# Kernel optimization log

Hardware: AMD Instinct MI355X
Metric: run time of the kernel (lower is better)

The kernel has to match this reference:

```python
import jax, jax.numpy as jnp
import numpy as np

WIDTH = 96
MODES = 42
LAYERS = 4
GROUPS = 6  # max(1, min(8, 96 // 16))
EPS = 1e-5
RESIDUAL_SCALE = 0.5


def _coord_grid(B, H, W, dtype):
    y = jnp.linspace(-1.0, 1.0, H, dtype=dtype)
    x = jnp.linspace(-1.0, 1.0, W, dtype=dtype)
    yy, xx = jnp.meshgrid(y, x, indexing='ij')
    grid = jnp.stack([xx, yy], axis=0)  # (2,H,W)
    return jnp.broadcast_to(grid[None], (B, 2, H, W))


def _spectral_conv(x, w):
    # x: (B,C,H,W) real; w: (Ci,Co,M,M,2) real
    B, C, H, W = x.shape
    xf = jnp.fft.rfft2(x)  # (B,C,H,W//2+1) complex
    Hm = min(MODES, H)
    Wm = min(MODES, W // 2 + 1)
    wc = (w[..., 0] + 1j * w[..., 1])[:, :, :Hm, :Wm]
    of = jnp.einsum('bihw,iohw->bohw', xf[:, :, :Hm, :Wm], wc)
    out_ft = jnp.zeros((B, w.shape[1], H, W // 2 + 1), dtype=of.dtype)
    out_ft = out_ft.at[:, :, :Hm, :Wm].set(of)
    return jnp.fft.irfft2(out_ft, s=(H, W))


def _conv1x1(x, w, b):
    # w: (Cout, Cin), b: (Cout,)
    return jnp.einsum('bihw,oi->bohw', x, w) + b[None, :, None, None]


def _depthwise3x3(x, w, b):
    # w: (C,1,3,3)
    y = jax.lax.conv_general_dilated(
        x, w, window_strides=(1, 1), padding=((1, 1), (1, 1)),
        dimension_numbers=('NCHW', 'OIHW', 'NCHW'),
        feature_group_count=x.shape[1])
    return y + b[None, :, None, None]


def _group_norm(x, g, b):
    B, C, H, W = x.shape
    xg = x.reshape(B, GROUPS, C // GROUPS, H, W)
    mean = jnp.mean(xg, axis=(2, 3, 4), keepdims=True)
    var = jnp.var(xg, axis=(2, 3, 4), keepdims=True)
    xn = ((xg - mean) * jax.lax.rsqrt(var + EPS)).reshape(B, C, H, W)
    return xn * g[None, :, None, None] + b[None, :, None, None]


def setup_inputs() -> dict:
    key = jax.random.key(0)
    ks = jax.random.split(key, 16)
    B, H, W = 8, 256, 256
    in_ch = 3 + 1 + 2
    scale = 1.0 / (WIDTH * WIDTH)
    inp = {
        'upsampled': jax.random.uniform(ks[0], (B, 3, H, W), dtype=jnp.float32),
        'noise': 0.1 * jax.random.normal(ks[1], (B, 1, H, W), dtype=jnp.float32),
        'in_proj_w': jax.random.normal(ks[2], (WIDTH, in_ch), dtype=jnp.float32) * (1.0 / np.sqrt(in_ch)),
        'in_proj_b': jnp.zeros((WIDTH,), dtype=jnp.float32),
        'spec_w': scale * jax.random.normal(ks[3], (WIDTH, WIDTH, MODES, MODES, 2), dtype=jnp.float32),
        'dense_w': jax.random.normal(ks[4], (LAYERS, WIDTH, WIDTH), dtype=jnp.float32) * (1.0 / np.sqrt(WIDTH)),
        'dense_b': jnp.zeros((LAYERS, WIDTH), dtype=jnp.float32),
        'local_w': jax.random.normal(ks[5], (LAYERS, WIDTH, 1, 3, 3), dtype=jnp.float32) * (1.0 / 3.0),
        'local_b': jnp.zeros((LAYERS, WIDTH), dtype=jnp.float32),
        'norm_g': jnp.ones((LAYERS, WIDTH), dtype=jnp.float32),
        'norm_b': jnp.zeros((LAYERS, WIDTH), dtype=jnp.float32),
        'out_proj_w': jax.random.normal(ks[6], (3, WIDTH), dtype=jnp.float32) * (1.0 / np.sqrt(WIDTH)),
        'out_proj_b': jnp.zeros((3,), dtype=jnp.float32),
    }
    return inp


def reference(upsampled, noise, in_proj_w, in_proj_b, spec_w, dense_w, dense_b,
              local_w, local_b, norm_g, norm_b, out_proj_w, out_proj_b):
    B, _, H, W = upsampled.shape
    grid = _coord_grid(B, H, W, upsampled.dtype)
    x = jnp.concatenate([upsampled, noise, grid], axis=1)
    x = jax.nn.gelu(_conv1x1(x, in_proj_w, in_proj_b), approximate=False)
    for l in range(LAYERS):
        delta = (_spectral_conv(x, spec_w)
                 + _conv1x1(x, dense_w[l], dense_b[l])
                 + _depthwise3x3(x, local_w[l], local_b[l]))
        x = x + RESIDUAL_SCALE * delta
        x = _group_norm(x, norm_g[l], norm_b[l])
        x = jax.nn.gelu(x, approximate=False)
    residual = _conv1x1(x, out_proj_w, out_proj_b)
    return jnp.clip(upsampled + residual, 0.0, 1.0)
```

## Files before the change

kernel.cpp:

```cpp
#include <hip/hip_runtime.h>
#include <math.h>

#define NHW 65536
#define PADM 1792
#define PI2 6.283185307179586f

__device__ __forceinline__ float gelu_f(float v) {
    return 0.5f * v * (1.0f + erff(v * 0.7071067811865476f));
}

__global__ void k_tables(float* __restrict__ D1, float* __restrict__ T1c, float* __restrict__ T1s,
                         float* __restrict__ T2c, float* __restrict__ T2s) {
    int idx = blockIdx.x * 256 + threadIdx.x;
    if (idx < 256 * 48) {
        int n = idx / 48, k = idx % 48;
        float ang = PI2 * (float)((n * k) & 255) / 256.0f;
        float s, c;
        sincosf(ang, &s, &c);
        D1[n * 96 + 2 * k] = c;
        D1[n * 96 + 2 * k + 1] = -s;
        T1c[n * 48 + k] = c;
        T1s[n * 48 + k] = s;
    }
    if (idx < 42 * 256) {
        int k = idx / 256, n = idx % 256;
        float ang = PI2 * (float)((n * k) & 255) / 256.0f;
        float s, c;
        sincosf(ang, &s, &c);
        T2c[idx] = c;
        T2s[idx] = s;
    }
}

__global__ void k_nrm_init(float2* __restrict__ nrm, int n) {
    int i = blockIdx.x * 256 + threadIdx.x;
    if (i < n) nrm[i] = make_float2(1.0f, 0.0f);
}

__global__ void __launch_bounds__(256) k_in(const float* __restrict__ up, const float* __restrict__ noise,
                                            const float* __restrict__ w, const float* __restrict__ bias,
                                            float* __restrict__ A, int b0) {
    __shared__ float ws_[96 * 6];
    __shared__ float bs_[96];
    int t = threadIdx.x;
    for (int i = t; i < 96 * 6; i += 256) ws_[i] = w[i];
    if (t < 96) bs_[t] = bias[t];
    __syncthreads();
    int br = blockIdx.x >> 8, h = blockIdx.x & 255;
    int b = b0 + br;
    float v0 = up[((size_t)(b * 3 + 0) * 256 + h) * 256 + t];
    float v1 = up[((size_t)(b * 3 + 1) * 256 + h) * 256 + t];
    float v2 = up[((size_t)(b * 3 + 2) * 256 + h) * 256 + t];
    float v3 = noise[((size_t)b * 256 + h) * 256 + t];
    float v4 = -1.0f + 2.0f * (float)t / 255.0f;
    float v5 = -1.0f + 2.0f * (float)h / 255.0f;
    size_t base = (size_t)br * 96 * NHW + (size_t)h * 256 + t;
    for (int o = 0; o < 96; o++) {
        const float* wo = ws_ + o * 6;
        float acc = bs_[o];
        acc = fmaf(v0, wo[0], acc); acc = fmaf(v1, wo[1], acc); acc = fmaf(v2, wo[2], acc);
        acc = fmaf(v3, wo[3], acc); acc = fmaf(v4, wo[4], acc); acc = fmaf(v5, wo[5], acc);
        A[base + (size_t)o * NHW] = acc;
    }
}

__global__ void __launch_bounds__(256) k_s1(const float* __restrict__ A, const float2* __restrict__ nrm,
                                            const float* __restrict__ D1, float* __restrict__ rz) {
    __shared__ float Xl[32][132];
    __shared__ float Dl[32][100];
    int t = threadIdx.x;
    int row0 = blockIdx.x * 128;
    int bc = blockIdx.x >> 1;
    float2 nv = nrm[bc];
    int tn = t % 16, tm = t / 16;
    int r0 = tn * 8, c0 = tm * 6;
    float acc[8][6] = {};
    for (int kc = 0; kc < 256; kc += 32) {
        __syncthreads();
#pragma unroll
        for (int it = 0; it < 4; it++) {
            int slot = t + 256 * it;
            int r = slot >> 3, j4 = (slot & 7) * 4;
            float4 g = *(const float4*)&A[(size_t)(row0 + r) * 256 + kc + j4];
            Xl[j4 + 0][r] = gelu_f(fmaf(g.x, nv.x, nv.y));
            Xl[j4 + 1][r] = gelu_f(fmaf(g.y, nv.x, nv.y));
            Xl[j4 + 2][r] = gelu_f(fmaf(g.z, nv.x, nv.y));
            Xl[j4 + 3][r] = gelu_f(fmaf(g.w, nv.x, nv.y));
        }
#pragma unroll
        for (int it = 0; it < 3; it++) {
            int slot = t + 256 * it;
            int rr = slot / 24, c4 = (slot % 24) * 4;
            *(float4*)&Dl[rr][c4] = *(const float4*)&D1[(size_t)(kc + rr) * 96 + c4];
        }
        __syncthreads();
        for (int k = 0; k < 32; k++) {
            float a[8], d[6];
#pragma unroll
            for (int i = 0; i < 8; i++) a[i] = Xl[k][r0 + i];
#pragma unroll
            for (int j = 0; j < 6; j++) d[j] = Dl[k][c0 + j];
#pragma unroll
            for (int i = 0; i < 8; i++)
#pragma unroll
                for (int j = 0; j < 6; j++) acc[i][j] = fmaf(a[i], d[j], acc[i][j]);
        }
    }
#pragma unroll
    for (int i = 0; i < 8; i++) {
        size_t row = row0 + r0 + i;
#pragma unroll
        for (int j = 0; j < 6; j++) {
            int col = c0 + j;
            if (col < 84) rz[row * 84 + col] = acc[i][j];
        }
    }
}

__global__ void __launch_bounds__(256) k_s2(const float* __restrict__ r1, const float* __restrict__ T1c,
                                            const float* __restrict__ T1s, float* __restrict__ xf) {
    int bc = blockIdx.x;
    int t = threadIdx.x;
    __shared__ float rl[32][88];
    __shared__ float tcl[32][48], tsl[32][48];
    int tkh = t / 11, tkw = t % 11;
    bool act = (t < 231);
    int kh0 = tkh * 2, kw0 = tkw * 4;
    float accr[2][4] = {}, acci[2][4] = {};
    const float* rp = r1 + (size_t)bc * 256 * 84;
    for (int hc = 0; hc < 256; hc += 32) {
        __syncthreads();
        for (int f = t; f < 32 * 88; f += 256) {
            int hl = f / 88, m = f % 88;
            rl[hl][m] = (m < 84) ? rp[(size_t)(hc + hl) * 84 + m] : 0.f;
        }
        for (int f = t; f < 32 * 48; f += 256) {
            int hl = f / 48, k = f % 48;
            tcl[hl][k] = T1c[(hc + hl) * 48 + k];
            tsl[hl][k] = T1s[(hc + hl) * 48 + k];
        }
        __syncthreads();
        if (act) {
            for (int hl = 0; hl < 32; hl++) {
                float c0 = tcl[hl][kh0], s0 = tsl[hl][kh0];
                float c1 = tcl[hl][kh0 + 1], s1v = tsl[hl][kh0 + 1];
#pragma unroll
                for (int j = 0; j < 4; j++) {
                    float arr = rl[hl][(kw0 + j) * 2], aii = rl[hl][(kw0 + j) * 2 + 1];
                    accr[0][j] = fmaf(arr, c0, fmaf(aii, s0, accr[0][j]));
                    acci[0][j] = fmaf(aii, c0, fmaf(-arr, s0, acci[0][j]));
                    accr[1][j] = fmaf(arr, c1, fmaf(aii, s1v, accr[1][j]));
                    acci[1][j] = fmaf(aii, c1, fmaf(-arr, s1v, acci[1][j]));
                }
            }
        }
    }
    if (act) {
        float* xp = xf + (size_t)bc * (PADM * 2);
#pragma unroll
        for (int i = 0; i < 2; i++)
#pragma unroll
            for (int j = 0; j < 4; j++) {
                int kw = kw0 + j;
                if (kw < 42) {
                    xp[((kh0 + i) * 42 + kw) * 2] = accr[i][j];
                    xp[((kh0 + i) * 42 + kw) * 2 + 1] = acci[i][j];
                }
            }
    }
}

__global__ void __launch_bounds__(256) k_s3(const float* __restrict__ xfb, const float* __restrict__ sw,
                                            float* __restrict__ ofb, int nbc) {
    int bx = blockIdx.x;
    int b = bx % nbc, mt = bx / nbc;
    int m0 = mt * 16;
    int t = threadIdx.x;
    __shared__ float2 xl[96][16];
    const float2* xx = (const float2*)xfb;
    for (int f = t; f < 1536; f += 256) {
        int i = f >> 4, ml = f & 15;
        int m = m0 + ml;
        float2 v = make_float2(0.f, 0.f);
        if (m < 1764) v = xx[(size_t)(b * 96 + i) * PADM + m];
        xl[i][ml] = v;
    }
    __syncthreads();
    int ml = t & 15, og = t >> 4;
    int m = m0 + ml;
    if (m >= 1764) return;
    float accr[6] = {}, acci[6] = {};
    const float2* wp = (const float2*)sw;
    for (int i = 0; i < 96; i++) {
        float2 xv = xl[i][ml];
#pragma unroll
        for (int j = 0; j < 6; j++) {
            int o = og * 6 + j;
            float2 wv = wp[(size_t)(i * 96 + o) * 1764 + m];
            accr[j] = fmaf(xv.x, wv.x, fmaf(-xv.y, wv.y, accr[j]));
            acci[j] = fmaf(xv.x, wv.y, fmaf(xv.y, wv.x, acci[j]));
        }
    }
    float2* op = (float2*)ofb;
#pragma unroll
    for (int j = 0; j < 6; j++) {
        int o = og * 6 + j;
        op[(size_t)(b * 96 + o) * PADM + m] = make_float2(accr[j], acci[j]);
    }
}

__global__ void __launch_bounds__(256) k_dense(const float* __restrict__ A, const float2* __restrict__ nrm,
                                               const float* __restrict__ dw, const float* __restrict__ db,
                                               float* __restrict__ B) {
    __shared__ float Xl[32][132];
    __shared__ float Wl[32][100];
    __shared__ float bs[96];
    __shared__ float2 ns[96];
    int t = threadIdx.x;
    int p0 = blockIdx.x * 128;
    int b = blockIdx.y;
    if (t < 96) { bs[t] = db[t]; ns[t] = nrm[b * 96 + t]; }
    int tn = t % 16, tm = t / 16;
    int n0 = tn * 8, m0 = tm * 6;
    float acc[8][6] = {};
    const float* xb = A + (size_t)b * 96 * NHW;
    for (int kc = 0; kc < 96; kc += 32) {
        __syncthreads();
#pragma unroll
        for (int it = 0; it < 4; it++) {
            int slot = t + 256 * it;
            int k = slot >> 5, j4 = (slot & 31) * 4;
            float4 g = *(const float4*)&xb[(size_t)(kc + k) * NHW + p0 + j4];
            float2 nv = ns[kc + k];
            Xl[k][j4 + 0] = gelu_f(fmaf(g.x, nv.x, nv.y));
            Xl[k][j4 + 1] = gelu_f(fmaf(g.y, nv.x, nv.y));
            Xl[k][j4 + 2] = gelu_f(fmaf(g.z, nv.x, nv.y));
            Xl[k][j4 + 3] = gelu_f(fmaf(g.w, nv.x, nv.y));
        }
#pragma unroll
        for (int it = 0; it < 3; it++) {
            int slot = t + 256 * it;
            int o = slot >> 3, j4 = (slot & 7) * 4;
            float4 g = *(const float4*)&dw[(size_t)o * 96 + kc + j4];
            Wl[j4 + 0][o] = g.x; Wl[j4 + 1][o] = g.y; Wl[j4 + 2][o] = g.z; Wl[j4 + 3][o] = g.w;
        }
        __syncthreads();
        for (int k = 0; k < 32; k++) {
            float a[8], wv[6];
#pragma unroll
            for (int i = 0; i < 8; i++) a[i] = Xl[k][n0 + i];
#pragma unroll
            for (int j = 0; j < 6; j++) wv[j] = Wl[k][m0 + j];
#pragma unroll
            for (int i = 0; i < 8; i++)
#pragma unroll
                for (int j = 0; j < 6; j++) acc[i][j] = fmaf(a[i], wv[j], acc[i][j]);
        }
    }
#pragma unroll
    for (int j = 0; j < 6; j++) {
        int o = m0 + j;
        float bv = bs[o];
        float* tp = B + ((size_t)b * 96 + o) * NHW + p0 + n0;
#pragma unroll
        for (int i = 0; i < 8; i++) tp[i] = acc[i][j] + bv;
    }
}

__global__ void __launch_bounds__(256) k_s5(const float* __restrict__ A, const float2* __restrict__ nrm,
                                            float* __restrict__ B, const float* __restrict__ ofb,
                                            const float* __restrict__ T2c, const float* __restrict__ T2s,
                                            const float* __restrict__ lw, const float* __restrict__ lb,
                                            float2* __restrict__ ps) {
    int bo = blockIdx.x;
    int o = bo % 96;
    int t = threadIdx.x;
    __shared__ float ofl[3528];
    __shared__ float xr[10][258];
    __shared__ float zl[8][84];
    __shared__ float rs1[4], rs2[4];
    float2 nv = nrm[bo];
    float Tc[42], Ts[42];
#pragma unroll
    for (int k = 0; k < 42; k++) { Tc[k] = T2c[k * 256 + t]; Ts[k] = T2s[k * 256 + t]; }
    float l9[9];
#pragma unroll
    for (int j = 0; j < 9; j++) l9[j] = lw[o * 9 + j];
    float lbv = lb[o];
    const float* xp = A + (size_t)bo * NHW;
    float* tp = B + (size_t)bo * NHW;
    const float* op_ = ofb + (size_t)bo * (PADM * 2);
    for (int f = t; f < 3528; f += 256) ofl[f] = op_[f];
    float s1 = 0.f, s2 = 0.f;
    for (int hc = 0; hc < 256; hc += 8) {
        __syncthreads();
        for (int f = t; f < 2580; f += 256) {
            int j = f / 258, cc = f % 258;
            int hr = hc - 1 + j, wc = cc - 1;
            float v = 0.f;
            if (hr >= 0 && hr < 256 && wc >= 0 && wc < 256)
                v = gelu_f(fmaf(xp[(size_t)hr * 256 + wc], nv.x, nv.y));
            xr[j][cc] = v;
        }
        for (int e = t; e < 336; e += 256) {
            int hl = e / 42, kw = e % 42;
            int h = hc + hl;
            float zr = 0.f, zi = 0.f;
            for (int kh = 0; kh < 42; kh++) {
                float c = T2c[kh * 256 + h], s = T2s[kh * 256 + h];
                float2 ov = *(const float2*)&ofl[(kh * 42 + kw) * 2];
                zr = fmaf(ov.x, c, fmaf(-ov.y, s, zr));
                zi = fmaf(ov.x, s, fmaf(ov.y, c, zi));
            }
            float fsc = (kw == 0) ? (1.0f / 65536.0f) : (2.0f / 65536.0f);
            zl[hl][2 * kw] = zr * fsc;
            zl[hl][2 * kw + 1] = zi * fsc;
        }
        __syncthreads();
#pragma unroll 1
        for (int hl = 0; hl < 8; hl++) {
            int h = hc + hl;
            float acc = 0.f;
#pragma unroll
            for (int k = 0; k < 42; k++) {
                acc = fmaf(zl[hl][2 * k], Tc[k], acc);
                acc = fmaf(-zl[hl][2 * k + 1], Ts[k], acc);
            }
            float dv = tp[(size_t)h * 256 + t];
            float dwv = lbv;
#pragma unroll
            for (int a = 0; a < 3; a++)
#pragma unroll
                for (int bq = 0; bq < 3; bq++) dwv = fmaf(xr[hl + a][t + bq], l9[a * 3 + bq], dwv);
            float xc = xr[hl + 1][t + 1];
            float val = xc + 0.5f * (acc + dv + dwv);
            tp[(size_t)h * 256 + t] = val;
            s1 += val;
            s2 = fmaf(val, val, s2);
        }
    }
    for (int off2 = 32; off2 > 0; off2 >>= 1) {
        s1 += __shfl_down(s1, off2);
        s2 += __shfl_down(s2, off2);
    }
    int wid = t >> 6, lane = t & 63;
    if (lane == 0) { rs1[wid] = s1; rs2[wid] = s2; }
    __syncthreads();
    if (t == 0) ps[bo] = make_float2(rs1[0] + rs1[1] + rs1[2] + rs1[3], rs2[0] + rs2[1] + rs2[2] + rs2[3]);
}

__global__ void k_stats(const float2* __restrict__ ps, const float* __restrict__ ng,
                        const float* __restrict__ nb, float2* __restrict__ nrm, int n) {
    int i = blockIdx.x * 64 + threadIdx.x;
    if (i >= n) return;
    int c = i % 96, b = i / 96, g = c >> 4;
    float s = 0.f, q = 0.f;
#pragma unroll
    for (int j = 0; j < 16; j++) { float2 v = ps[b * 96 + g * 16 + j]; s += v.x; q += v.y; }
    const float inv_n = 1.0f / 1048576.0f;
    float mean = s * inv_n;
    float var = q * inv_n - mean * mean;
    float rstd = rsqrtf(var + 1e-5f);
    float sc = rstd * ng[c];
    nrm[i] = make_float2(sc, nb[c] - mean * sc);
}

__global__ void __launch_bounds__(256) k_out(const float* __restrict__ A, const float2* __restrict__ nrm,
                                             const float* __restrict__ up, const float* __restrict__ opw,
                                             const float* __restrict__ opb, float* __restrict__ out, int b0) {
    __shared__ float wl[288];
    __shared__ float2 nl[96];
    int t = threadIdx.x;
    int br = blockIdx.x >> 8;
    if (t < 96) nl[t] = nrm[br * 96 + t];
    for (int f = t; f < 288; f += 256) wl[f] = opw[f];
    __syncthreads();
    int p = (blockIdx.x & 255) * 256 + t;
    const float* xp = A + (size_t)br * 96 * NHW + p;
    float a0 = opb[0], a1 = opb[1], a2 = opb[2];
    for (int i = 0; i < 96; i++) {
        float2 nv = nl[i];
        float xv = gelu_f(fmaf(xp[(size_t)i * NHW], nv.x, nv.y));
        a0 = fmaf(xv, wl[i], a0);
        a1 = fmaf(xv, wl[96 + i], a1);
        a2 = fmaf(xv, wl[192 + i], a2);
    }
    int b = b0 + br;
#pragma unroll
    for (int o = 0; o < 3; o++) {
        float av = (o == 0) ? a0 : ((o == 1) ? a1 : a2);
        size_t idx = ((size_t)b * 3 + o) * NHW + p;
        float v = up[idx] + av;
        out[idx] = fminf(fmaxf(v, 0.0f), 1.0f);
    }
}

extern "C" void kernel_launch(void* const* d_in, const int* in_sizes, int n_in,
                              void* d_out, int out_size, void* d_ws, size_t ws_size,
                              hipStream_t stream) {
    const float* up = (const float*)d_in[0];
    const float* noise = (const float*)d_in[1];
    const float* ipw = (const float*)d_in[2];
    const float* ipb = (const float*)d_in[3];
    const float* specw = (const float*)d_in[4];
    const float* dw = (const float*)d_in[5];
    const float* db = (const float*)d_in[6];
    const float* lw = (const float*)d_in[7];
    const float* lb = (const float*)d_in[8];
    const float* ng = (const float*)d_in[9];
    const float* nb = (const float*)d_in[10];
    const float* opw = (const float*)d_in[11];
    const float* opb = (const float*)d_in[12];
    float* out = (float*)d_out;

    auto needf = [](size_t nbc) -> size_t {
        return nbc * (2ull * 6291456 + 2064384 + 2ull * 344064 + 3ull * 192) + 70656ull;
    };
    int nbc = 8;
    while (nbc > 1 && needf(nbc) * 4ull > ws_size) nbc >>= 1;
    if (needf(nbc) * 4ull > ws_size) return;

    float* ws = (float*)d_ws;
    float* A0  = ws;
    float* B0  = A0 + (size_t)nbc * 6291456;
    float* rz  = B0 + (size_t)nbc * 6291456;
    float* xfb = rz + (size_t)nbc * 2064384;
    float* ofb = xfb + (size_t)nbc * 344064;
    float* ps  = ofb + (size_t)nbc * 344064;
    float* nrm0 = ps + (size_t)nbc * 192;
    float* nrm1 = nrm0 + (size_t)nbc * 192;
    float* D1  = nrm1 + (size_t)nbc * 192;
    float* T1c = D1 + 24576;
    float* T1s = T1c + 12288;
    float* T2c = T1s + 12288;
    float* T2s = T2c + 10752;

    k_tables<<<48, 256, 0, stream>>>(D1, T1c, T1s, T2c, T2s);

    for (int b0 = 0; b0 < 8; b0 += nbc) {
        k_nrm_init<<<(nbc * 96 + 255) / 256, 256, 0, stream>>>((float2*)nrm0, nbc * 96);
        k_in<<<nbc * 256, 256, 0, stream>>>(up, noise, ipw, ipb, A0, b0);
        float *A = A0, *B = B0, *nc = nrm0, *nn = nrm1;
        for (int l = 0; l < 4; l++) {
            k_s1<<<nbc * 192, 256, 0, stream>>>(A, (const float2*)nc, D1, rz);
            k_s2<<<nbc * 96, 256, 0, stream>>>(rz, T1c, T1s, xfb);
            k_s3<<<111 * nbc, 256, 0, stream>>>(xfb, specw, ofb, nbc);
            k_dense<<<dim3(512, nbc), 256, 0, stream>>>(A, (const float2*)nc,
                                                        dw + (size_t)l * 9216, db + (size_t)l * 96, B);
            k_s5<<<nbc * 96, 256, 0, stream>>>(A, (const float2*)nc, B, ofb, T2c, T2s,
                                               lw + (size_t)l * 864, lb + (size_t)l * 96, (float2*)ps);
            k_stats<<<(nbc * 96 + 63) / 64, 64, 0, stream>>>((const float2*)ps, ng + (size_t)l * 96,
                                                             nb + (size_t)l * 96, (float2*)nn, nbc * 96);
            float* tA = A; A = B; B = tA;
            float* tN = nc; nc = nn; nn = tN;
        }
        k_out<<<nbc * 256, 256, 0, stream>>>(A, (const float2*)nc, up, opw, opb, out, b0);
    }
}
```

Before: 5.592 ms.

## Materialize activated tensor once per layer and split inverse-DFT kernel by rows

Replaces the lazy norm+GELU applied inside each consumer (s1, dense, s5, out) with a separate k_act pass that writes the activated tensor once per layer. k_s5 is split into two blocks per plane, loads the halo with float4, and replaces the per-thread twiddle tables with a Chebyshev recurrence, which lowers register pressure and table loads. k_stats is updated to sum the doubled partials. The trade-off is an extra full read and write of the activation tensor per layer in exchange for removing repeated erf evaluations in several kernels, and the recurrence adds a small accumulated rounding error.

```diff
diff --git a/kernel.cpp b/kernel.cpp
--- a/kernel.cpp
+++ b/kernel.cpp
@@ -32,14 +32,9 @@
     }
 }
 
-__global__ void k_nrm_init(float2* __restrict__ nrm, int n) {
-    int i = blockIdx.x * 256 + threadIdx.x;
-    if (i < n) nrm[i] = make_float2(1.0f, 0.0f);
-}
-
 __global__ void __launch_bounds__(256) k_in(const float* __restrict__ up, const float* __restrict__ noise,
                                             const float* __restrict__ w, const float* __restrict__ bias,
-                                            float* __restrict__ A, int b0) {
+                                            float* __restrict__ X, int b0) {
     __shared__ float ws_[96 * 6];
     __shared__ float bs_[96];
     int t = threadIdx.x;
@@ -60,18 +55,16 @@
         float acc = bs_[o];
         acc = fmaf(v0, wo[0], acc); acc = fmaf(v1, wo[1], acc); acc = fmaf(v2, wo[2], acc);
         acc = fmaf(v3, wo[3], acc); acc = fmaf(v4, wo[4], acc); acc = fmaf(v5, wo[5], acc);
-        A[base + (size_t)o * NHW] = acc;
-    }
-}
-
-__global__ void __launch_bounds__(256) k_s1(const float* __restrict__ A, const float2* __restrict__ nrm,
-                                            const float* __restrict__ D1, float* __restrict__ rz) {
+        X[base + (size_t)o * NHW] = gelu_f(acc);
+    }
+}
+
+__global__ void __launch_bounds__(256) k_s1(const float* __restrict__ X, const float* __restrict__ D1,
+                                            float* __restrict__ rz) {
     __shared__ float Xl[32][132];
     __shared__ float Dl[32][100];
     int t = threadIdx.x;
     int row0 = blockIdx.x * 128;
-    int bc = blockIdx.x >> 1;
-    float2 nv = nrm[bc];
     int tn = t % 16, tm = t / 16;
     int r0 = tn * 8, c0 = tm * 6;
     float acc[8][6] = {};
@@ -81,11 +74,8 @@
         for (int it = 0; it < 4; it++) {
             int slot = t + 256 * it;
             int r = slot >> 3, j4 = (slot & 7) * 4;
-            float4 g = *(const float4*)&A[(size_t)(row0 + r) * 256 + kc + j4];
-            Xl[j4 + 0][r] = gelu_f(fmaf(g.x, nv.x, nv.y));
-            Xl[j4 + 1][r] = gelu_f(fmaf(g.y, nv.x, nv.y));
-            Xl[j4 + 2][r] = gelu_f(fmaf(g.z, nv.x, nv.y));
-            Xl[j4 + 3][r] = gelu_f(fmaf(g.w, nv.x, nv.y));
+            float4 g = *(const float4*)&X[(size_t)(row0 + r) * 256 + kc + j4];
+            Xl[j4 + 0][r] = g.x; Xl[j4 + 1][r] = g.y; Xl[j4 + 2][r] = g.z; Xl[j4 + 3][r] = g.w;
         }
 #pragma unroll
         for (int it = 0; it < 3; it++) {
@@ -209,33 +199,26 @@
     }
 }
 
-__global__ void __launch_bounds__(256) k_dense(const float* __restrict__ A, const float2* __restrict__ nrm,
-                                               const float* __restrict__ dw, const float* __restrict__ db,
-                                               float* __restrict__ B) {
+__global__ void __launch_bounds__(256) k_dense(const float* __restrict__ X, const float* __restrict__ dw,
+                                               const float* __restrict__ db, float* __restrict__ B) {
     __shared__ float Xl[32][132];
     __shared__ float Wl[32][100];
     __shared__ float bs[96];
-    __shared__ float2 ns[96];
     int t = threadIdx.x;
     int p0 = blockIdx.x * 128;
     int b = blockIdx.y;
-    if (t < 96) { bs[t] = db[t]; ns[t] = nrm[b * 96 + t]; }
+    if (t < 96) bs[t] = db[t];
     int tn = t % 16, tm = t / 16;
     int n0 = tn * 8, m0 = tm * 6;
     float acc[8][6] = {};
-    const float* xb = A + (size_t)b * 96 * NHW;
+    const float* xb = X + (size_t)b * 96 * NHW;
     for (int kc = 0; kc < 96; kc += 32) {
         __syncthreads();
 #pragma unroll
         for (int it = 0; it < 4; it++) {
             int slot = t + 256 * it;
             int k = slot >> 5, j4 = (slot & 31) * 4;
-            float4 g = *(const float4*)&xb[(size_t)(kc + k) * NHW + p0 + j4];
-            float2 nv = ns[kc + k];
-            Xl[k][j4 + 0] = gelu_f(fmaf(g.x, nv.x, nv.y));
-            Xl[k][j4 + 1] = gelu_f(fmaf(g.y, nv.x, nv.y));
-            Xl[k][j4 + 2] = gelu_f(fmaf(g.z, nv.x, nv.y));
-            Xl[k][j4 + 3] = gelu_f(fmaf(g.w, nv.x, nv.y));
+            *(float4*)&Xl[k][j4] = *(const float4*)&xb[(size_t)(kc + k) * NHW + p0 + j4];
         }
 #pragma unroll
         for (int it = 0; it < 3; it++) {
@@ -267,72 +250,84 @@
     }
 }
 
-__global__ void __launch_bounds__(256) k_s5(const float* __restrict__ A, const float2* __restrict__ nrm,
-                                            float* __restrict__ B, const float* __restrict__ ofb,
+__global__ void __launch_bounds__(256) k_s5(const float* __restrict__ X, float* __restrict__ B,
+                                            const float* __restrict__ ofb,
                                             const float* __restrict__ T2c, const float* __restrict__ T2s,
                                             const float* __restrict__ lw, const float* __restrict__ lb,
                                             float2* __restrict__ ps) {
-    int bo = blockIdx.x;
-    int o = bo % 96;
+    int bid = blockIdx.x;
+    int plane = bid >> 1, half = bid & 1;
+    int o = plane % 96;
     int t = threadIdx.x;
     __shared__ float ofl[3528];
-    __shared__ float xr[10][258];
+    __shared__ float xr[10][264];
     __shared__ float zl[8][84];
     __shared__ float rs1[4], rs2[4];
-    float2 nv = nrm[bo];
-    float Tc[42], Ts[42];
-#pragma unroll
-    for (int k = 0; k < 42; k++) { Tc[k] = T2c[k * 256 + t]; Ts[k] = T2s[k * 256 + t]; }
     float l9[9];
 #pragma unroll
     for (int j = 0; j < 9; j++) l9[j] = lw[o * 9 + j];
     float lbv = lb[o];
-    const float* xp = A + (size_t)bo * NHW;
-    float* tp = B + (size_t)bo * NHW;
-    const float* op_ = ofb + (size_t)bo * (PADM * 2);
+    const float* xp = X + (size_t)plane * NHW;
+    float* tp = B + (size_t)plane * NHW;
+    const float* op_ = ofb + (size_t)plane * (PADM * 2);
     for (int f = t; f < 3528; f += 256) ofl[f] = op_[f];
+    if (t < 20) xr[t >> 1][(t & 1) ? 260 : 3] = 0.f;
+    float cw1 = T2c[256 + t], sw1 = T2s[256 + t];
     float s1 = 0.f, s2 = 0.f;
-    for (int hc = 0; hc < 256; hc += 8) {
-        __syncthreads();
-        for (int f = t; f < 2580; f += 256) {
-            int j = f / 258, cc = f % 258;
-            int hr = hc - 1 + j, wc = cc - 1;
-            float v = 0.f;
-            if (hr >= 0 && hr < 256 && wc >= 0 && wc < 256)
-                v = gelu_f(fmaf(xp[(size_t)hr * 256 + wc], nv.x, nv.y));
-            xr[j][cc] = v;
+    int h0 = half * 128;
+    for (int hc = h0; hc < h0 + 128; hc += 8) {
+        __syncthreads();
+        for (int f = t; f < 640; f += 256) {
+            int j = f >> 6, q = (f & 63) * 4;
+            int hr = hc - 1 + j;
+            float4 g = make_float4(0.f, 0.f, 0.f, 0.f);
+            if (hr >= 0 && hr < 256) g = *(const float4*)&xp[(size_t)hr * 256 + q];
+            *(float4*)&xr[j][4 + q] = g;
         }
         for (int e = t; e < 336; e += 256) {
             int hl = e / 42, kw = e % 42;
             int h = hc + hl;
-            float zr = 0.f, zi = 0.f;
-            for (int kh = 0; kh < 42; kh++) {
-                float c = T2c[kh * 256 + h], s = T2s[kh * 256 + h];
-                float2 ov = *(const float2*)&ofl[(kh * 42 + kw) * 2];
-                zr = fmaf(ov.x, c, fmaf(-ov.y, s, zr));
-                zi = fmaf(ov.x, s, fmaf(ov.y, c, zi));
+            float c1 = T2c[256 + h], s1v = T2s[256 + h];
+            float twoc = 2.f * c1;
+            float cp = 1.f, cc = c1, sp = 0.f, sc = s1v;
+            float2 ov = *(const float2*)&ofl[kw * 2];
+            float zr = ov.x, zi = ov.y;
+#pragma unroll
+            for (int kh = 1; kh < 42; kh++) {
+                ov = *(const float2*)&ofl[(kh * 42 + kw) * 2];
+                zr = fmaf(ov.x, cc, fmaf(-ov.y, sc, zr));
+                zi = fmaf(ov.x, sc, fmaf(ov.y, cc, zi));
+                float cn = fmaf(twoc, cc, -cp); cp = cc; cc = cn;
+                float sn = fmaf(twoc, sc, -sp); sp = sc; sc = sn;
             }
             float fsc = (kw == 0) ? (1.0f / 65536.0f) : (2.0f / 65536.0f);
             zl[hl][2 * kw] = zr * fsc;
             zl[hl][2 * kw + 1] = zi * fsc;
         }
         __syncthreads();
+        float twoc = 2.f * cw1;
 #pragma unroll 1
         for (int hl = 0; hl < 8; hl++) {
             int h = hc + hl;
-            float acc = 0.f;
-#pragma unroll
-            for (int k = 0; k < 42; k++) {
-                acc = fmaf(zl[hl][2 * k], Tc[k], acc);
-                acc = fmaf(-zl[hl][2 * k + 1], Ts[k], acc);
+            float2 z0 = *(const float2*)&zl[hl][0];
+            float acc0 = z0.x, acc1 = 0.f;
+            float cp = 1.f, cc = cw1, sp = 0.f, sc = sw1;
+#pragma unroll
+            for (int k = 1; k < 42; k++) {
+                float2 zz = *(const float2*)&zl[hl][2 * k];
+                if (k & 1) acc1 = fmaf(zz.x, cc, fmaf(-zz.y, sc, acc1));
+                else       acc0 = fmaf(zz.x, cc, fmaf(-zz.y, sc, acc0));
+                float cn = fmaf(twoc, cc, -cp); cp = cc; cc = cn;
+                float sn = fmaf(twoc, sc, -sp); sp = sc; sc = sn;
             }
+            float acc = acc0 + acc1;
             float dv = tp[(size_t)h * 256 + t];
             float dwv = lbv;
 #pragma unroll
             for (int a = 0; a < 3; a++)
 #pragma unroll
-                for (int bq = 0; bq < 3; bq++) dwv = fmaf(xr[hl + a][t + bq], l9[a * 3 + bq], dwv);
-            float xc = xr[hl + 1][t + 1];
+                for (int bq = 0; bq < 3; bq++) dwv = fmaf(xr[hl + a][3 + t + bq], l9[a * 3 + bq], dwv);
+            float xc = xr[hl + 1][4 + t];
             float val = xc + 0.5f * (acc + dv + dwv);
             tp[(size_t)h * 256 + t] = val;
             s1 += val;
@@ -346,7 +341,7 @@
     int wid = t >> 6, lane = t & 63;
     if (lane == 0) { rs1[wid] = s1; rs2[wid] = s2; }
     __syncthreads();
-    if (t == 0) ps[bo] = make_float2(rs1[0] + rs1[1] + rs1[2] + rs1[3], rs2[0] + rs2[1] + rs2[2] + rs2[3]);
+    if (t == 0) ps[bid] = make_float2(rs1[0] + rs1[1] + rs1[2] + rs1[3], rs2[0] + rs2[1] + rs2[2] + rs2[3]);
 }
 
 __global__ void k_stats(const float2* __restrict__ ps, const float* __restrict__ ng,
@@ -355,8 +350,9 @@
     if (i >= n) return;
     int c = i % 96, b = i / 96, g = c >> 4;
     float s = 0.f, q = 0.f;
-#pragma unroll
-    for (int j = 0; j < 16; j++) { float2 v = ps[b * 96 + g * 16 + j]; s += v.x; q += v.y; }
+    int base = (b * 96 + g * 16) * 2;
+#pragma unroll
+    for (int j = 0; j < 32; j++) { float2 v = ps[base + j]; s += v.x; q += v.y; }
     const float inv_n = 1.0f / 1048576.0f;
     float mean = s * inv_n;
     float var = q * inv_n - mean * mean;
@@ -365,22 +361,35 @@
     nrm[i] = make_float2(sc, nb[c] - mean * sc);
 }
 
-__global__ void __launch_bounds__(256) k_out(const float* __restrict__ A, const float2* __restrict__ nrm,
-                                             const float* __restrict__ up, const float* __restrict__ opw,
-                                             const float* __restrict__ opb, float* __restrict__ out, int b0) {
+__global__ void __launch_bounds__(256) k_act(const float* __restrict__ V, const float2* __restrict__ nrm,
+                                             float* __restrict__ X, int total4) {
+    int idx = blockIdx.x * 256 + threadIdx.x;
+    int stride = gridDim.x * 256;
+    for (; idx < total4; idx += stride) {
+        float2 nv = nrm[idx >> 14];
+        float4 v = ((const float4*)V)[idx];
+        float4 r;
+        r.x = gelu_f(fmaf(v.x, nv.x, nv.y));
+        r.y = gelu_f(fmaf(v.y, nv.x, nv.y));
+        r.z = gelu_f(fmaf(v.z, nv.x, nv.y));
+        r.w = gelu_f(fmaf(v.w, nv.x, nv.y));
+        ((float4*)X)[idx] = r;
+    }
+}
+
+__global__ void __launch_bounds__(256) k_out(const float* __restrict__ X, const float* __restrict__ up,
+                                             const float* __restrict__ opw, const float* __restrict__ opb,
+                                             float* __restrict__ out, int b0) {
     __shared__ float wl[288];
-    __shared__ float2 nl[96];
     int t = threadIdx.x;
     int br = blockIdx.x >> 8;
-    if (t < 96) nl[t] = nrm[br * 96 + t];
     for (int f = t; f < 288; f += 256) wl[f] = opw[f];
     __syncthreads();
     int p = (blockIdx.x & 255) * 256 + t;
-    const float* xp = A + (size_t)br * 96 * NHW + p;
+    const float* xp = X + (size_t)br * 96 * NHW + p;
     float a0 = opb[0], a1 = opb[1], a2 = opb[2];
     for (int i = 0; i < 96; i++) {
-        float2 nv = nl[i];
-        float xv = gelu_f(fmaf(xp[(size_t)i * NHW], nv.x, nv.y));
+        float xv = xp[(size_t)i * NHW];
         a0 = fmaf(xv, wl[i], a0);
         a1 = fmaf(xv, wl[96 + i], a1);
         a2 = fmaf(xv, wl[192 + i], a2);
@@ -414,22 +423,21 @@
     float* out = (float*)d_out;
 
     auto needf = [](size_t nbc) -> size_t {
-        return nbc * (2ull * 6291456 + 2064384 + 2ull * 344064 + 3ull * 192) + 70656ull;
+        return nbc * (2ull * 6291456 + 2064384 + 2ull * 344064 + 384 + 192) + 70656ull;
     };
     int nbc = 8;
     while (nbc > 1 && needf(nbc) * 4ull > ws_size) nbc >>= 1;
     if (needf(nbc) * 4ull > ws_size) return;
 
     float* ws = (float*)d_ws;
-    float* A0  = ws;
-    float* B0  = A0 + (size_t)nbc * 6291456;
-    float* rz  = B0 + (size_t)nbc * 6291456;
+    float* X   = ws;
+    float* B   = X + (size_t)nbc * 6291456;
+    float* rz  = B + (size_t)nbc * 6291456;
     float* xfb = rz + (size_t)nbc * 2064384;
     float* ofb = xfb + (size_t)nbc * 344064;
     float* ps  = ofb + (size_t)nbc * 344064;
-    float* nrm0 = ps + (size_t)nbc * 192;
-    float* nrm1 = nrm0 + (size_t)nbc * 192;
-    float* D1  = nrm1 + (size_t)nbc * 192;
+    float* nrm = ps + (size_t)nbc * 384;
+    float* D1  = nrm + (size_t)nbc * 192;
     float* T1c = D1 + 24576;
     float* T1s = T1c + 12288;
     float* T2c = T1s + 12288;
@@ -438,22 +446,18 @@
     k_tables<<<48, 256, 0, stream>>>(D1, T1c, T1s, T2c, T2s);
 
     for (int b0 = 0; b0 < 8; b0 += nbc) {
-        k_nrm_init<<<(nbc * 96 + 255) / 256, 256, 0, stream>>>((float2*)nrm0, nbc * 96);
-        k_in<<<nbc * 256, 256, 0, stream>>>(up, noise, ipw, ipb, A0, b0);
-        float *A = A0, *B = B0, *nc = nrm0, *nn = nrm1;
+        k_in<<<nbc * 256, 256, 0, stream>>>(up, noise, ipw, ipb, X, b0);
         for (int l = 0; l < 4; l++) {
-            k_s1<<<nbc * 192, 256, 0, stream>>>(A, (const float2*)nc, D1, rz);
+            k_s1<<<nbc * 192, 256, 0, stream>>>(X, D1, rz);
             k_s2<<<nbc * 96, 256, 0, stream>>>(rz, T1c, T1s, xfb);
             k_s3<<<111 * nbc, 256, 0, stream>>>(xfb, specw, ofb, nbc);
-            k_dense<<<dim3(512, nbc), 256, 0, stream>>>(A, (const float2*)nc,
-                                                        dw + (size_t)l * 9216, db + (size_t)l * 96, B);
-            k_s5<<<nbc * 96, 256, 0, stream>>>(A, (const float2*)nc, B, ofb, T2c, T2s,
-                                               lw + (size_t)l * 864, lb + (size_t)l * 96, (float2*)ps);
+            k_dense<<<dim3(512, nbc), 256, 0, stream>>>(X, dw + (size_t)l * 9216, db + (size_t)l * 96, B);
+            k_s5<<<nbc * 192, 256, 0, stream>>>(X, B, ofb, T2c, T2s,
+                                                lw + (size_t)l * 864, lb + (size_t)l * 96, (float2*)ps);
             k_stats<<<(nbc * 96 + 63) / 64, 64, 0, stream>>>((const float2*)ps, ng + (size_t)l * 96,
-                                                             nb + (size_t)l * 96, (float2*)nn, nbc * 96);
-            float* tA = A; A = B; B = tA;
-            float* tN = nc; nc = nn; nn = tN;
-        }
-        k_out<<<nbc * 256, 256, 0, stream>>>(A, (const float2*)nc, up, opw, opb, out, b0);
-    }
-}
+                                                             nb + (size_t)l * 96, (float2*)nrm, nbc * 96);
+            k_act<<<4096, 256, 0, stream>>>(B, (const float2*)nrm, X, nbc * 96 * 16384);
+        }
+        k_out<<<nbc * 256, 256, 0, stream>>>(X, up, opw, opb, out, b0);
+    }
+}
```

After: 4.537 ms. 18.9% less time.
